# Optimization experiments

Measured on AMD Instinct MI355X. Metric: run time of the kernel, lower is better.

## Reference

```python
import jax, jax.numpy as jnp
import numpy as np

V, D, NH, T_MAX, L, MLP = 50257, 1024, 16, 1024, 12, 4
HD = D // NH
F = D * MLP
B, T = 2, 1024


def setup_inputs() -> dict:
    key = jax.random.key(0)
    ks = jax.random.split(key, 16)
    s = 0.02
    inp = {
        'tokens': jax.random.randint(ks[0], (B, T), 0, V, dtype=jnp.int32),
        'wte': jax.random.normal(ks[1], (V, D), jnp.float32) * s,
        'wpe': jax.random.normal(ks[2], (T_MAX, D), jnp.float32) * s,
        'ln1_w': jnp.ones((L, D)), 'ln1_b': jnp.zeros((L, D)),
        'attn_w': jax.random.normal(ks[3], (L, D, 3 * D), jnp.float32) * s,
        'attn_b': jnp.zeros((L, 3 * D)),
        'aproj_w': jax.random.normal(ks[4], (L, D, D), jnp.float32) * s,
        'aproj_b': jnp.zeros((L, D)),
        'ln2_w': jnp.ones((L, D)), 'ln2_b': jnp.zeros((L, D)),
        'fc_w': jax.random.normal(ks[5], (L, D, F), jnp.float32) * s,
        'fc_b': jnp.zeros((L, F)),
        'proj_w': jax.random.normal(ks[6], (L, F, D), jnp.float32) * s,
        'proj_b': jnp.zeros((L, D)),
        'lnf_w': jnp.ones((D,)), 'lnf_b': jnp.zeros((D,)),
    }
    return inp


def _ln(x, w, b, eps=1e-5):
    m = jnp.mean(x, -1, keepdims=True)
    v = jnp.var(x, -1, keepdims=True)
    return (x - m) * jax.lax.rsqrt(v + eps) * w + b


def _forward(tokens, wte, wpe, ln1_w, ln1_b, attn_w, attn_b, aproj_w, aproj_b,
             ln2_w, ln2_b, fc_w, fc_b, proj_w, proj_b, lnf_w, lnf_b):
    b, t = tokens.shape
    x = wte[tokens] + wpe[:t]  # [B,T,D]
    scale = HD ** -0.5
    causal = jnp.tril(jnp.ones((t, t), bool))  # [T,T]

    def block(x, p):
        l1w, l1b, aw, ab, apw, apb, l2w, l2b, fw, fb, pw, pb = p
        h = _ln(x, l1w, l1b)
        qkv = h @ aw + ab  # [B,T,3D]
        q, k, v = jnp.split(qkv, 3, axis=-1)
        # rearrange 'b t (h n) -> b n t h' with n=NH: last dim is (head_size, n_heads)
        def split_heads(u):
            return u.reshape(b, t, HD, NH).transpose(0, 3, 1, 2)  # [B,NH,T,HD]
        q, k, v = split_heads(q), split_heads(k), split_heads(v)
        scores = jnp.einsum('bnth,bnsh->bnts', q, k) * scale
        scores = jnp.where(causal, scores, -jnp.inf)
        w = jax.nn.softmax(scores, axis=-1)
        att = jnp.einsum('bnts,bnsh->bnth', w, v)
        # rearrange 'b n t h -> b t (n h)'
        att = att.transpose(0, 2, 1, 3).reshape(b, t, D)
        x = x + (att @ apw + apb)
        h2 = _ln(x, l2w, l2b)
        x = x + (jax.nn.gelu(h2 @ fw + fb, approximate=False) @ pw + pb)
        return x, None

    params = (ln1_w, ln1_b, attn_w, attn_b, aproj_w, aproj_b,
              ln2_w, ln2_b, fc_w, fc_b, proj_w, proj_b)
    x, _ = jax.lax.scan(block, x, params)
    x = _ln(x, lnf_w, lnf_b)[:, -1:, :]  # [B,1,D]
    return x @ wte.T  # tied lm_head -> [B,1,V]


def reference(tokens, wte, wpe, ln1_w, ln1_b, attn_w, attn_b, aproj_w, aproj_b,
              ln2_w, ln2_b, fc_w, fc_b, proj_w, proj_b, lnf_w, lnf_b):
    return _forward(tokens, wte, wpe, ln1_w, ln1_b, attn_w, attn_b, aproj_w,
                    aproj_b, ln2_w, ln2_b, fc_w, fc_b, proj_w, proj_b, lnf_w, lnf_b)
```

## Files before the change

### kernel.cpp

```cpp
#include <hip/hip_runtime.h>
#include <cstdint>
#include <math.h>


using u16 = unsigned short;
using bf16x8 = __attribute__((ext_vector_type(8))) short;
using f32x4 = __attribute__((ext_vector_type(4))) float;

#define GLDS16(g, l)                                                        \
  __builtin_amdgcn_global_load_lds(                                         \
      (const __attribute__((address_space(1))) void*)(g),                   \
      (__attribute__((address_space(3))) void*)(l), 16, 0, 0)

__device__ __forceinline__ u16 f2bf(float f) {
  union { float f; unsigned u; } t; t.f = f;
  unsigned r = t.u + 0x7fffu + ((t.u >> 16) & 1u);
  return (u16)(r >> 16);
}

__device__ __forceinline__ float fast_erf(float x) {
  float ax = fabsf(x);
  float t = 1.f / (1.f + 0.3275911f * ax);
  float y = t * (0.254829592f +
            t * (-0.284496736f +
            t * (1.421413741f +
            t * (-1.453152027f +
            t * 1.061405429f))));
  float r = 1.f - y * __expf(-ax * ax);
  return copysignf(r, x);
}

#define DD 1024
#define TTT 1024
#define MR 2048
#define FFF 4096
#define VVV 50257

__global__ __launch_bounds__(256) void k_embed(const int* __restrict__ tokens,
                                               const float* __restrict__ wte,
                                               const float* __restrict__ wpe,
                                               float* __restrict__ x) {
  int m = blockIdx.x, d = threadIdx.x * 4;
  int t = m & (TTT - 1);
  int tok = tokens[m];
  const float4 a = *(const float4*)(wte + (size_t)tok * DD + d);
  const float4 p = *(const float4*)(wpe + (size_t)t * DD + d);
  float4 o; o.x = a.x + p.x; o.y = a.y + p.y; o.z = a.z + p.z; o.w = a.w + p.w;
  *(float4*)(x + (size_t)m * DD + d) = o;
}

__global__ __launch_bounds__(256) void k_ln(const float* __restrict__ x,
                                            const float* __restrict__ w,
                                            const float* __restrict__ b,
                                            u16* __restrict__ out) {
  const int wid = threadIdx.x >> 6, lane = threadIdx.x & 63;
  const int m = blockIdx.x * 4 + wid;
  const float* row = x + (size_t)m * DD;
  float4 v[4];
  float s = 0.f, q = 0.f;
#pragma unroll
  for (int j = 0; j < 4; ++j) {
    v[j] = *(const float4*)(row + j * 256 + lane * 4);
    s += v[j].x + v[j].y + v[j].z + v[j].w;
    q += v[j].x * v[j].x + v[j].y * v[j].y + v[j].z * v[j].z + v[j].w * v[j].w;
  }
#pragma unroll
  for (int off = 1; off < 64; off <<= 1) { s += __shfl_xor(s, off); q += __shfl_xor(q, off); }
  float mean = s * (1.f / DD);
  float var = q * (1.f / DD) - mean * mean;
  float rs = rsqrtf(var + 1e-5f);
#pragma unroll
  for (int j = 0; j < 4; ++j) {
    const float4 wv = *(const float4*)(w + j * 256 + lane * 4);
    const float4 bv = *(const float4*)(b + j * 256 + lane * 4);
    u16 o[4];
    o[0] = f2bf((v[j].x - mean) * rs * wv.x + bv.x);
    o[1] = f2bf((v[j].y - mean) * rs * wv.y + bv.y);
    o[2] = f2bf((v[j].z - mean) * rs * wv.z + bv.z);
    o[3] = f2bf((v[j].w - mean) * rs * wv.w + bv.w);
    *(uint64_t*)(out + (size_t)m * DD + j * 256 + lane * 4) = *(uint64_t*)o;
  }
}

__global__ __launch_bounds__(256) void k_wtrans2(const float* __restrict__ atw,
                                                 const float* __restrict__ apw,
                                                 const float* __restrict__ fcw,
                                                 const float* __restrict__ pjw,
                                                 u16* __restrict__ wt) {
  __shared__ u16 tb[64][72];
  const int id = blockIdx.x;
  const float* W; u16* Wt; int K, N, local, kts;
  if (id < 768)       { W = atw; Wt = wt;           K = 1024; N = 3072; local = id;        kts = 4; }
  else if (id < 1024) { W = apw; Wt = wt + 3145728; K = 1024; N = 1024; local = id - 768;  kts = 4; }
  else if (id < 2048) { W = fcw; Wt = wt + 4194304; K = 1024; N = 4096; local = id - 1024; kts = 4; }
  else                { W = pjw; Wt = wt + 8388608; K = 4096; N = 1024; local = id - 2048; kts = 6; }
  const int k0 = (local & ((1 << kts) - 1)) * 64, n0 = (local >> kts) * 64;
  const int tid = threadIdx.x;
  const int rr = tid >> 4, c4 = (tid & 15) * 4;
#pragma unroll
  for (int i = 0; i < 4; ++i) {
    const int r = rr + i * 16;
    const float4 v = *(const float4*)(W + (size_t)(k0 + r) * N + n0 + c4);
    tb[c4 + 0][r] = f2bf(v.x);
    tb[c4 + 1][r] = f2bf(v.y);
    tb[c4 + 2][r] = f2bf(v.z);
    tb[c4 + 3][r] = f2bf(v.w);
  }
  __syncthreads();
  const int n = tid >> 3, k8 = (tid & 7) * 8;
#pragma unroll
  for (int s = 0; s < 2; ++s) {
    u16 o[8];
#pragma unroll
    for (int j = 0; j < 8; ++j) o[j] = tb[n + s * 32][k8 + j];
    *(bf16x8*)(Wt + (size_t)(n0 + n + s * 32) * K + k0 + k8) = *(bf16x8*)o;
  }
}

template <int EPI>
__global__ __launch_bounds__(256) void k_gemm(const u16* __restrict__ A,
                                              const u16* __restrict__ Bt,
                                              const float* __restrict__ bias,
                                              u16* __restrict__ outb,
                                              float* __restrict__ xres,
                                              int M, int N, int K, int KC) {
  __shared__ u16 As[2][128 * 64];
  __shared__ u16 Bs[2][128 * 64];
  const int nbx = gridDim.x, nby = gridDim.y;
  const int nwg = nbx * nby * gridDim.z;
  const int orig = blockIdx.x + nbx * (blockIdx.y + nby * blockIdx.z);
  const int qq = nwg >> 3, rr = nwg & 7;
  const int xcd = orig & 7, pos = orig >> 3;
  const int wg = (xcd < rr ? xcd * (qq + 1) : rr * (qq + 1) + (xcd - rr) * qq) + pos;
  const int bx = wg % nbx;
  const int tmpw = wg / nbx;
  const int by = tmpw % nby, bz = tmpw / nby;

  const int tid = threadIdx.x;
  const int lane = tid & 63, wid = tid >> 6;
  const int wr = wid >> 1, wc = wid & 1;
  const int l15 = lane & 15, l4 = lane >> 4;
  const int sx = l15 & 7;
  const int m0 = bx * 128, n0 = by * 128;
  f32x4 acc[4][4] = {};

  const int srow = tid >> 3;
  const int scol = (((tid & 7) ^ (srow & 7)) * 8);
  const int k0beg = bz * KC;
  const int nt = KC >> 6;

  const u16* Ap = A + (size_t)(m0 + srow) * K + scol;
  const u16* Bp = Bt + (size_t)(n0 + srow) * K + scol;

#define STAGE(buf, k0)                                                      \
  {                                                                         \
    _Pragma("unroll")                                                       \
    for (int it = 0; it < 4; ++it) {                                        \
      GLDS16(Ap + (size_t)it * 32 * K + (k0), (char*)As[buf] + it * 4096 + tid * 16); \
      GLDS16(Bp + (size_t)it * 32 * K + (k0), (char*)Bs[buf] + it * 4096 + tid * 16); \
    }                                                                       \
  }

  STAGE(0, k0beg);
  for (int t = 0; t < nt; ++t) {
    if (t + 1 < nt) {
      STAGE((t + 1) & 1, k0beg + (t + 1) * 64);
      asm volatile("s_waitcnt vmcnt(8)" ::: "memory");
    } else {
      asm volatile("s_waitcnt vmcnt(0)" ::: "memory");
    }
    __builtin_amdgcn_sched_barrier(0);
    __builtin_amdgcn_s_barrier();
    __builtin_amdgcn_sched_barrier(0);
    const u16* Ab = As[t & 1];
    const u16* Bb = Bs[t & 1];
#pragma unroll
    for (int ks = 0; ks < 2; ++ks) {
      const int ch = ((ks * 4 + l4) ^ sx) * 8;
      bf16x8 af[4], bfr[4];
#pragma unroll
      for (int i = 0; i < 4; ++i)
        af[i] = *(const bf16x8*)(Ab + (wr * 64 + i * 16 + l15) * 64 + ch);
#pragma unroll
      for (int j = 0; j < 4; ++j)
        bfr[j] = *(const bf16x8*)(Bb + (wc * 64 + j * 16 + l15) * 64 + ch);
      __builtin_amdgcn_s_setprio(1);
#pragma unroll
      for (int i = 0; i < 4; ++i)
#pragma unroll
        for (int j = 0; j < 4; ++j)
          acc[i][j] = __builtin_amdgcn_mfma_f32_16x16x32_bf16(af[i], bfr[j], acc[i][j], 0, 0, 0);
      __builtin_amdgcn_s_setprio(0);
    }
    __builtin_amdgcn_sched_barrier(0);
    __builtin_amdgcn_s_barrier();
    __builtin_amdgcn_sched_barrier(0);
  }
#undef STAGE
#pragma unroll
  for (int j = 0; j < 4; ++j) {
    const int col = n0 + wc * 64 + j * 16 + l15;
    const float bs = (EPI == 3 && bz != 0) ? 0.f : bias[col];
#pragma unroll
    for (int i = 0; i < 4; ++i) {
#pragma unroll
      for (int r = 0; r < 4; ++r) {
        const int row = m0 + wr * 64 + i * 16 + l4 * 4 + r;
        float v = acc[i][j][r] + bs;
        if (EPI == 0) {
          outb[(size_t)row * N + col] = f2bf(v);
        } else if (EPI == 2) {
          float g = 0.5f * v * (1.f + fast_erf(v * 0.70710678118f));
          outb[(size_t)row * N + col] = f2bf(g);
        } else {
          atomicAdd(&xres[(size_t)row * N + col], v);
        }
      }
    }
  }
}

__global__ __launch_bounds__(256) void k_repack(const u16* __restrict__ qkv,
                                                u16* __restrict__ Kb,
                                                u16* __restrict__ Vt) {
  __shared__ u16 tile[16 * 1024];
  const int tid = threadIdx.x;
  const int m0 = blockIdx.x * 16;
  const int part = blockIdx.y + 1;
  const int b = m0 >> 10;
  const int tg0 = m0 & (TTT - 1);
#pragma unroll
  for (int p = 0; p < 8; ++p) {
    int row = p * 2 + (tid >> 7);
    int col8 = (tid & 127) * 8;
    bf16x8 v = *(const bf16x8*)(qkv + (size_t)(m0 + row) * 3072 + part * 1024 + col8);
    int e = col8 ^ (((col8 >> 4) & 7) << 3);
    *(bf16x8*)(tile + row * 1024 + e) = v;
  }
  __syncthreads();
  const int lane = tid & 63, wid = tid >> 6;
  if (part == 1) {
    for (int p = wid; p < 256; p += 4) {
      int t = p >> 4, n = p & 15;
      int e = (lane * 16 + n) ^ ((lane & 7) << 3);
      u16 val = tile[t * 1024 + e];
      Kb[(((size_t)(b * 16 + n)) * TTT + tg0 + t) * 64 + lane] = val;
    }
  } else {
    for (int p = wid; p < 32; p += 4) {
      int n = p >> 1, tc = p & 1;
      int e = (lane * 16 + n) ^ ((lane & 7) << 3);
      u16 val8[8];
#pragma unroll
      for (int k = 0; k < 8; ++k) val8[k] = tile[(tc * 8 + k) * 1024 + e];
      *(bf16x8*)(Vt + (((size_t)(b * 16 + n)) * 64 + lane) * TTT + tg0 + tc * 8) =
          *(bf16x8*)val8;
    }
  }
}

__global__ __launch_bounds__(256) void k_attn(const u16* __restrict__ qkv,
                                              const u16* __restrict__ Kb,
                                              const u16* __restrict__ Vt,
                                              u16* __restrict__ attout) {
  __shared__ u16 Ks[128 * 64];
  __shared__ u16 Vs[64 * 128];
  __shared__ u16 Ps[4][16 * 136];

  const int tid = threadIdx.x;
  const int lane = tid & 63, wid = tid >> 6;
  const int l15 = lane & 15, l4 = lane >> 4;
  const int bn = blockIdx.x;
  const int b = bn >> 4, nh = bn & 15;
  const char* Kg0 = (const char*)(Kb + (size_t)bn * TTT * 64);
  const char* Vg0 = (const char*)(Vt + (size_t)bn * 64 * TTT);

#pragma unroll
  for (int pass = 0; pass < 2; ++pass) {
    const int qtr = pass == 0 ? 15 - (int)blockIdx.y : (int)blockIdx.y;
    const int q0 = qtr * 64;

    const int qrow = q0 + wid * 16 + l15;
    const u16* qsrc = qkv + (size_t)(b * TTT + qrow) * 3072 + nh;
    bf16x8 aq[2];
#pragma unroll
    for (int ks = 0; ks < 2; ++ks) {
      short tmp[8];
#pragma unroll
      for (int j = 0; j < 8; ++j) tmp[j] = (short)qsrc[(ks * 32 + l4 * 8 + j) * 16];
      aq[ks] = *(bf16x8*)tmp;
    }

    float m_run[4], l_part[4];
    f32x4 o[4] = {};
#pragma unroll
    for (int r = 0; r < 4; ++r) { m_run[r] = -1e30f; l_part[r] = 0.f; }

    const int ntk = (qtr >> 1) + 1;
    for (int kt = 0; kt < ntk; ++kt) {
#pragma unroll
      for (int it = 0; it < 4; ++it) {
        int L = it * 4096 + tid * 16;
        int Ls = L ^ (((L >> 7) & 7) << 4);
        GLDS16(Kg0 + (size_t)kt * 16384 + Ls, (char*)Ks + L);
      }
#pragma unroll
      for (int it = 0; it < 4; ++it) {
        int L = it * 4096 + tid * 16;
        int Ls = L ^ (((L >> 8) & 7) << 4);
        int hrow = Ls >> 8, cb = Ls & 255;
        GLDS16(Vg0 + (size_t)hrow * 2048 + kt * 256 + cb, (char*)Vs + L);
      }
      __syncthreads();

      f32x4 sf[8];
#pragma unroll
      for (int cf = 0; cf < 8; ++cf) {
        f32x4 z = {};
#pragma unroll
        for (int ks = 0; ks < 2; ++ks) {
          int P = (cf * 16 + l15) * 128 + (ks * 32 + l4 * 8) * 2;
          bf16x8 kb = *(const bf16x8*)((const char*)Ks + (P ^ (((P >> 7) & 7) << 4)));
          z = __builtin_amdgcn_mfma_f32_16x16x32_bf16(aq[ks], kb, z, 0, 0, 0);
        }
        sf[cf] = z;
      }
      const bool lastkt = (kt == ntk - 1);
#pragma unroll
      for (int cf = 0; cf < 8; ++cf)
#pragma unroll
        for (int r = 0; r < 4; ++r) {
          float s = sf[cf][r] * 0.125f;
          if (lastkt) {
            int kg = kt * 128 + cf * 16 + l15;
            int qg = q0 + wid * 16 + l4 * 4 + r;
            if (kg > qg) s = -1e30f;
          }
          sf[cf][r] = s;
        }
      float fac[4];
#pragma unroll
      for (int r = 0; r < 4; ++r) {
        float tm = sf[0][r];
#pragma unroll
        for (int cf = 1; cf < 8; ++cf) tm = fmaxf(tm, sf[cf][r]);
#pragma unroll
        for (int off = 1; off < 16; off <<= 1) tm = fmaxf(tm, __shfl_xor(tm, off));
        float mnew = fmaxf(m_run[r], tm);
        fac[r] = __expf(m_run[r] - mnew);
        m_run[r] = mnew;
        float ps = 0.f;
#pragma unroll
        for (int cf = 0; cf < 8; ++cf) {
          float p = __expf(sf[cf][r] - mnew);
          sf[cf][r] = p;
          ps += p;
        }
        l_part[r] = l_part[r] * fac[r] + ps;
      }
#pragma unroll
      for (int cf = 0; cf < 8; ++cf)
#pragma unroll
        for (int r = 0; r < 4; ++r)
          Ps[wid][(l4 * 4 + r) * 136 + cf * 16 + l15] = f2bf(sf[cf][r]);
#pragma unroll
      for (int hf = 0; hf < 4; ++hf)
#pragma unroll
        for (int r = 0; r < 4; ++r) o[hf][r] *= fac[r];
      bf16x8 pa[4];
#pragma unroll
      for (int ks = 0; ks < 4; ++ks)
        pa[ks] = *(const bf16x8*)&Ps[wid][l15 * 136 + ks * 32 + l4 * 8];
#pragma unroll
      for (int hf = 0; hf < 4; ++hf) {
#pragma unroll
        for (int ks = 0; ks < 4; ++ks) {
          int P = (hf * 16 + l15) * 256 + (ks * 32 + l4 * 8) * 2;
          bf16x8 vb = *(const bf16x8*)((const char*)Vs + (P ^ (((P >> 8) & 7) << 4)));
          o[hf] = __builtin_amdgcn_mfma_f32_16x16x32_bf16(pa[ks], vb, o[hf], 0, 0, 0);
        }
      }
      __syncthreads();
    }
    float lsum[4];
#pragma unroll
    for (int r = 0; r < 4; ++r) {
      float s = l_part[r];
#pragma unroll
      for (int off = 1; off < 16; off <<= 1) s += __shfl_xor(s, off);
      lsum[r] = s;
    }
#pragma unroll
    for (int hf = 0; hf < 4; ++hf)
#pragma unroll
      for (int r = 0; r < 4; ++r) {
        float val = o[hf][r] / lsum[r];
        size_t row = (size_t)b * TTT + q0 + wid * 16 + l4 * 4 + r;
        attout[row * DD + nh * 64 + hf * 16 + l15] = f2bf(val);
      }
  }
}

__global__ __launch_bounds__(256) void k_head(const float* __restrict__ x,
                                              const float* __restrict__ lnf_w,
                                              const float* __restrict__ lnf_b,
                                              const float* __restrict__ wte,
                                              float* __restrict__ out) {
  __shared__ float xs[2 * DD];
  __shared__ float sm[8];
  int tid = threadIdx.x;
  int wid = tid >> 6, lane = tid & 63;
#pragma unroll
  for (int bb = 0; bb < 2; ++bb) {
    int m = bb * TTT + (TTT - 1);
    const float4 v = *(const float4*)(x + (size_t)m * DD + tid * 4);
    float s = v.x + v.y + v.z + v.w;
    float q = v.x * v.x + v.y * v.y + v.z * v.z + v.w * v.w;
#pragma unroll
    for (int off = 1; off < 64; off <<= 1) { s += __shfl_xor(s, off); q += __shfl_xor(q, off); }
    if ((tid & 63) == 0) { sm[wid] = s; sm[4 + wid] = q; }
    __syncthreads();
    s = sm[0] + sm[1] + sm[2] + sm[3];
    q = sm[4] + sm[5] + sm[6] + sm[7];
    float mean = s * (1.f / DD);
    float var = q * (1.f / DD) - mean * mean;
    float rs = rsqrtf(var + 1e-5f);
    const float4 wv = *(const float4*)(lnf_w + tid * 4);
    const float4 bv = *(const float4*)(lnf_b + tid * 4);
    float4 o;
    o.x = (v.x - mean) * rs * wv.x + bv.x;
    o.y = (v.y - mean) * rs * wv.y + bv.y;
    o.z = (v.z - mean) * rs * wv.z + bv.z;
    o.w = (v.w - mean) * rs * wv.w + bv.w;
    *(float4*)(xs + bb * DD + tid * 4) = o;
    __syncthreads();
  }
  for (int v = blockIdx.x * 4 + wid; v < VVV; v += gridDim.x * 4) {
    const float* wr = wte + (size_t)v * DD;
    float a0 = 0.f, a1 = 0.f;
#pragma unroll
    for (int j = 0; j < 4; ++j) {
      const float4 wv = *(const float4*)(wr + lane * 16 + j * 4);
      const float4 x0 = *(const float4*)(xs + lane * 16 + j * 4);
      const float4 x1 = *(const float4*)(xs + DD + lane * 16 + j * 4);
      a0 += wv.x * x0.x + wv.y * x0.y + wv.z * x0.z + wv.w * x0.w;
      a1 += wv.x * x1.x + wv.y * x1.y + wv.z * x1.z + wv.w * x1.w;
    }
#pragma unroll
    for (int off = 1; off < 64; off <<= 1) { a0 += __shfl_xor(a0, off); a1 += __shfl_xor(a1, off); }
    if (lane == 0) { out[v] = a0; out[VVV + v] = a1; }
  }
}

extern "C" void kernel_launch(void* const* d_in, const int* in_sizes, int n_in,
                              void* d_out, int out_size, void* d_ws, size_t ws_size,
                              hipStream_t stream) {
  const int* tokens    = (const int*)d_in[0];
  const float* wte     = (const float*)d_in[1];
  const float* wpe     = (const float*)d_in[2];
  const float* ln1_w   = (const float*)d_in[3];
  const float* ln1_b   = (const float*)d_in[4];
  const float* attn_w  = (const float*)d_in[5];
  const float* attn_b  = (const float*)d_in[6];
  const float* aproj_w = (const float*)d_in[7];
  const float* aproj_b = (const float*)d_in[8];
  const float* ln2_w   = (const float*)d_in[9];
  const float* ln2_b   = (const float*)d_in[10];
  const float* fc_w    = (const float*)d_in[11];
  const float* fc_b    = (const float*)d_in[12];
  const float* proj_w  = (const float*)d_in[13];
  const float* proj_b  = (const float*)d_in[14];
  const float* lnf_w   = (const float*)d_in[15];
  const float* lnf_b   = (const float*)d_in[16];

  char* ws = (char*)d_ws;
  float* x    = (float*)(ws);
  u16* h      = (u16*)(ws + (8u << 20));
  u16* wt     = (u16*)(ws + (12u << 20));
  u16* qkv    = (u16*)(ws + (36u << 20));
  u16* Kb     = (u16*)(ws + (48u << 20));
  u16* Vt     = (u16*)(ws + (52u << 20));
  u16* attb   = (u16*)(ws + (56u << 20));
  u16* mlph   = (u16*)(ws + (36u << 20));
  float* out  = (float*)d_out;

  u16* atw = wt;
  u16* apw = wt + 3145728;
  u16* fcw = wt + 4194304;
  u16* pjw = wt + 8388608;

  k_embed<<<MR, 256, 0, stream>>>(tokens, wte, wpe, x);

  for (int l = 0; l < 12; ++l) {
    k_wtrans2<<<3072, 256, 0, stream>>>(attn_w + (size_t)l * DD * 3 * DD,
                                        aproj_w + (size_t)l * DD * DD,
                                        fc_w + (size_t)l * DD * FFF,
                                        proj_w + (size_t)l * FFF * DD, wt);
    k_ln<<<MR / 4, 256, 0, stream>>>(x, ln1_w + l * DD, ln1_b + l * DD, h);
    k_gemm<0><<<dim3(16, 24, 1), 256, 0, stream>>>(h, atw, attn_b + (size_t)l * 3 * DD, qkv, nullptr, MR, 3072, 1024, 1024);
    k_repack<<<dim3(128, 2), 256, 0, stream>>>(qkv, Kb, Vt);
    k_attn<<<dim3(32, 8), 256, 0, stream>>>(qkv, Kb, Vt, attb);
    k_gemm<3><<<dim3(16, 8, 2), 256, 0, stream>>>(attb, apw, aproj_b + (size_t)l * DD, nullptr, x, MR, 1024, 1024, 512);
    k_ln<<<MR / 4, 256, 0, stream>>>(x, ln2_w + l * DD, ln2_b + l * DD, h);
    k_gemm<2><<<dim3(16, 32, 1), 256, 0, stream>>>(h, fcw, fc_b + (size_t)l * FFF, mlph, nullptr, MR, 4096, 1024, 1024);
    k_gemm<3><<<dim3(16, 8, 4), 256, 0, stream>>>(mlph, pjw, proj_b + (size_t)l * DD, nullptr, x, MR, 1024, 4096, 1024);
  }
  k_head<<<512, 256, 0, stream>>>(x, lnf_w, lnf_b, wte, out);
}
```

Baseline: 2.103 ms.

## Replace split-K atomics with partial buffers reduced in fused add-LayerNorm kernels

The split-K projection GEMMs now write per-slice fp32 partial results to a scratch buffer instead of issuing atomicAdd into the residual stream. The following LayerNorm kernel, or the head kernel, sums those partials into the residual, writes it back and normalises in the same pass. The per-layer weight transpose/convert is also merged with the first LayerNorm into one combined launch. This removes atomic contention and one launch per layer, at the cost of extra partial-buffer traffic (up to four 8MB buffers read back).

```diff
diff --git a/kernel.cpp b/kernel.cpp
--- a/kernel.cpp
+++ b/kernel.cpp
@@ -49,18 +49,24 @@
   *(float4*)(x + (size_t)m * DD + d) = o;
 }
 
-__global__ __launch_bounds__(256) void k_ln(const float* __restrict__ x,
-                                            const float* __restrict__ w,
-                                            const float* __restrict__ b,
-                                            u16* __restrict__ out) {
+__device__ __forceinline__ void addln_body(float* __restrict__ x,
+                                           const float* __restrict__ pp, int npart,
+                                           const float* __restrict__ w,
+                                           const float* __restrict__ b,
+                                           u16* __restrict__ out, int blk) {
   const int wid = threadIdx.x >> 6, lane = threadIdx.x & 63;
-  const int m = blockIdx.x * 4 + wid;
-  const float* row = x + (size_t)m * DD;
+  const int m = blk * 4 + wid;
+  float* row = x + (size_t)m * DD;
   float4 v[4];
   float s = 0.f, q = 0.f;
 #pragma unroll
   for (int j = 0; j < 4; ++j) {
     v[j] = *(const float4*)(row + j * 256 + lane * 4);
+    for (int p = 0; p < npart; ++p) {
+      const float4 pv = *(const float4*)(pp + (size_t)p * MR * DD + (size_t)m * DD + j * 256 + lane * 4);
+      v[j].x += pv.x; v[j].y += pv.y; v[j].z += pv.z; v[j].w += pv.w;
+    }
+    if (npart) *(float4*)(row + j * 256 + lane * 4) = v[j];
     s += v[j].x + v[j].y + v[j].z + v[j].w;
     q += v[j].x * v[j].x + v[j].y * v[j].y + v[j].z * v[j].z + v[j].w * v[j].w;
   }
@@ -82,13 +88,20 @@
   }
 }
 
-__global__ __launch_bounds__(256) void k_wtrans2(const float* __restrict__ atw,
-                                                 const float* __restrict__ apw,
-                                                 const float* __restrict__ fcw,
-                                                 const float* __restrict__ pjw,
-                                                 u16* __restrict__ wt) {
+__global__ __launch_bounds__(256) void k_addln(float* __restrict__ x,
+                                               const float* __restrict__ pp, int npart,
+                                               const float* __restrict__ w,
+                                               const float* __restrict__ b,
+                                               u16* __restrict__ out) {
+  addln_body(x, pp, npart, w, b, out, blockIdx.x);
+}
+
+__device__ __forceinline__ void wtrans_body(const float* __restrict__ atw,
+                                            const float* __restrict__ apw,
+                                            const float* __restrict__ fcw,
+                                            const float* __restrict__ pjw,
+                                            u16* __restrict__ wt, int id) {
   __shared__ u16 tb[64][72];
-  const int id = blockIdx.x;
   const float* W; u16* Wt; int K, N, local, kts;
   if (id < 768)       { W = atw; Wt = wt;           K = 1024; N = 3072; local = id;        kts = 4; }
   else if (id < 1024) { W = apw; Wt = wt + 3145728; K = 1024; N = 1024; local = id - 768;  kts = 4; }
@@ -117,12 +130,29 @@
   }
 }
 
+__global__ __launch_bounds__(256) void k_prep(float* __restrict__ x,
+                                              const float* __restrict__ pp, int npart,
+                                              const float* __restrict__ w,
+                                              const float* __restrict__ b,
+                                              u16* __restrict__ out,
+                                              const float* __restrict__ atw,
+                                              const float* __restrict__ apw,
+                                              const float* __restrict__ fcw,
+                                              const float* __restrict__ pjw,
+                                              u16* __restrict__ wt) {
+  if (blockIdx.x < 512) {
+    addln_body(x, pp, npart, w, b, out, blockIdx.x);
+  } else {
+    wtrans_body(atw, apw, fcw, pjw, wt, blockIdx.x - 512);
+  }
+}
+
 template <int EPI>
 __global__ __launch_bounds__(256) void k_gemm(const u16* __restrict__ A,
                                               const u16* __restrict__ Bt,
                                               const float* __restrict__ bias,
                                               u16* __restrict__ outb,
-                                              float* __restrict__ xres,
+                                              float* __restrict__ pp,
                                               int M, int N, int K, int KC) {
   __shared__ u16 As[2][128 * 64];
   __shared__ u16 Bs[2][128 * 64];
@@ -197,10 +227,11 @@
     __builtin_amdgcn_sched_barrier(0);
   }
 #undef STAGE
+  float* ppz = (EPI == 4) ? pp + (size_t)bz * M * N : nullptr;
 #pragma unroll
   for (int j = 0; j < 4; ++j) {
     const int col = n0 + wc * 64 + j * 16 + l15;
-    const float bs = (EPI == 3 && bz != 0) ? 0.f : bias[col];
+    const float bs = (EPI == 4 && bz != 0) ? 0.f : bias[col];
 #pragma unroll
     for (int i = 0; i < 4; ++i) {
 #pragma unroll
@@ -213,7 +244,7 @@
           float g = 0.5f * v * (1.f + fast_erf(v * 0.70710678118f));
           outb[(size_t)row * N + col] = f2bf(g);
         } else {
-          atomicAdd(&xres[(size_t)row * N + col], v);
+          ppz[(size_t)row * N + col] = v;
         }
       }
     }
@@ -402,6 +433,7 @@
 }
 
 __global__ __launch_bounds__(256) void k_head(const float* __restrict__ x,
+                                              const float* __restrict__ pp, int npart,
                                               const float* __restrict__ lnf_w,
                                               const float* __restrict__ lnf_b,
                                               const float* __restrict__ wte,
@@ -413,7 +445,11 @@
 #pragma unroll
   for (int bb = 0; bb < 2; ++bb) {
     int m = bb * TTT + (TTT - 1);
-    const float4 v = *(const float4*)(x + (size_t)m * DD + tid * 4);
+    float4 v = *(const float4*)(x + (size_t)m * DD + tid * 4);
+    for (int p = 0; p < npart; ++p) {
+      const float4 pv = *(const float4*)(pp + (size_t)p * MR * DD + (size_t)m * DD + tid * 4);
+      v.x += pv.x; v.y += pv.y; v.z += pv.z; v.w += pv.w;
+    }
     float s = v.x + v.y + v.z + v.w;
     float q = v.x * v.x + v.y * v.y + v.z * v.z + v.w * v.w;
 #pragma unroll
@@ -482,6 +518,7 @@
   u16* Vt     = (u16*)(ws + (52u << 20));
   u16* attb   = (u16*)(ws + (56u << 20));
   u16* mlph   = (u16*)(ws + (36u << 20));
+  float* pp   = (float*)(ws + (60u << 20));
   float* out  = (float*)d_out;
 
   u16* atw = wt;
@@ -492,18 +529,19 @@
   k_embed<<<MR, 256, 0, stream>>>(tokens, wte, wpe, x);
 
   for (int l = 0; l < 12; ++l) {
-    k_wtrans2<<<3072, 256, 0, stream>>>(attn_w + (size_t)l * DD * 3 * DD,
-                                        aproj_w + (size_t)l * DD * DD,
-                                        fc_w + (size_t)l * DD * FFF,
-                                        proj_w + (size_t)l * FFF * DD, wt);
-    k_ln<<<MR / 4, 256, 0, stream>>>(x, ln1_w + l * DD, ln1_b + l * DD, h);
+    k_prep<<<3584, 256, 0, stream>>>(x, pp, l == 0 ? 0 : 4,
+                                     ln1_w + l * DD, ln1_b + l * DD, h,
+                                     attn_w + (size_t)l * DD * 3 * DD,
+                                     aproj_w + (size_t)l * DD * DD,
+                                     fc_w + (size_t)l * DD * FFF,
+                                     proj_w + (size_t)l * FFF * DD, wt);
     k_gemm<0><<<dim3(16, 24, 1), 256, 0, stream>>>(h, atw, attn_b + (size_t)l * 3 * DD, qkv, nullptr, MR, 3072, 1024, 1024);
     k_repack<<<dim3(128, 2), 256, 0, stream>>>(qkv, Kb, Vt);
     k_attn<<<dim3(32, 8), 256, 0, stream>>>(qkv, Kb, Vt, attb);
-    k_gemm<3><<<dim3(16, 8, 2), 256, 0, stream>>>(attb, apw, aproj_b + (size_t)l * DD, nullptr, x, MR, 1024, 1024, 512);
-    k_ln<<<MR / 4, 256, 0, stream>>>(x, ln2_w + l * DD, ln2_b + l * DD, h);
+    k_gemm<4><<<dim3(16, 8, 2), 256, 0, stream>>>(attb, apw, aproj_b + (size_t)l * DD, nullptr, pp, MR, 1024, 1024, 512);
+    k_addln<<<512, 256, 0, stream>>>(x, pp, 2, ln2_w + l * DD, ln2_b + l * DD, h);
     k_gemm<2><<<dim3(16, 32, 1), 256, 0, stream>>>(h, fcw, fc_b + (size_t)l * FFF, mlph, nullptr, MR, 4096, 1024, 1024);
-    k_gemm<3><<<dim3(16, 8, 4), 256, 0, stream>>>(mlph, pjw, proj_b + (size_t)l * DD, nullptr, x, MR, 1024, 4096, 1024);
-  }
-  k_head<<<512, 256, 0, stream>>>(x, lnf_w, lnf_b, wte, out);
-}
+    k_gemm<4><<<dim3(16, 8, 4), 256, 0, stream>>>(mlph, pjw, proj_b + (size_t)l * DD, nullptr, pp, MR, 1024, 4096, 1024);
+  }
+  k_head<<<512, 256, 0, stream>>>(x, pp, 4, lnf_w, lnf_b, wte, out);
+}
```

New measurement: 1.921 ms. 1.09x faster.
